# Optimization experiments

Hardware: AMD Instinct MI355X
Metric: run time of the kernel (lower is better)

## Reference

```python
import jax, jax.numpy as jnp
import numpy as np
from jax import lax

B, T = 16384, 1000


def setup_inputs() -> dict:
    key = jax.random.key(0)
    k1, k2, k3, k4 = jax.random.split(key, 4)
    xicovs = jax.random.normal(k1, (B, T, 2, 2), dtype=jnp.float32) * 0.1
    dy = jax.random.normal(k2, (B, T, 2), dtype=jnp.float32) * 0.1
    coeffs_A = jax.random.normal(k3, (2, 2), dtype=jnp.float32) * 0.05
    C = jax.random.normal(k4, (2, 2), dtype=jnp.float32)
    x0 = jnp.zeros((B, 2), dtype=jnp.float32)
    dt = jnp.ones((1,), dtype=jnp.float32) * 0.001
    return {"xicovs": xicovs, "dy": dy, "coeffs_A": coeffs_A, "C": C, "x0": x0, "dt": dt}


def reference(xicovs, dy, coeffs_A, C, x0, dt):
    """Unrolls the GaussianDynamics recurrent cell over T steps with lax.scan.

    Per step (faithful to the original call):
      A_m  = coeffs_A - xicov @ C                     # [B,2,2]
      out  = (C @ x_prev) * dt                        # emitted output
      x    = x_prev + (A_m @ x_prev) * dt + xicov @ dy_t
    Returns (outputs [B,T,2], final_state [B,2]).
    """
    dts = dt[0]

    def step(x, inp):
        xic, dyt = inp  # [B,2,2], [B,2]
        A_m = coeffs_A - jnp.einsum('bij,jk->bik', xic, C)
        out = jnp.einsum('ij,bj->bi', C, x) * dts
        x_new = x + jnp.einsum('bij,bj->bi', A_m, x) * dts + jnp.einsum('bij,bj->bi', xic, dyt)
        return x_new, out

    xs = (jnp.moveaxis(xicovs, 1, 0), jnp.moveaxis(dy, 1, 0))  # time-major
    x_final, outs = lax.scan(step, x0, xs)
    return jnp.moveaxis(outs, 0, 1), x_final
```

## Files before the change

kernel.cpp:

```cpp
#include <hip/hip_runtime.h>


constexpr int BATCH = 16384;
constexpr int TLEN  = 1000;
constexpr int TPB   = 256;
constexpr int SPT   = 4;

typedef float vfloat4 __attribute__((ext_vector_type(4)));
typedef float vfloat2 __attribute__((ext_vector_type(2)));

template <int CTRL, int ROWMASK>
__device__ __forceinline__ float dppf(float oldv, float srcv) {
    return __int_as_float(__builtin_amdgcn_update_dpp(
        __float_as_int(oldv), __float_as_int(srcv), CTRL, ROWMASK, 0xf, false));
}

__global__ __launch_bounds__(TPB, 8) void gd_scan_kernel(
    const float* __restrict__ xicovs,
    const float* __restrict__ dyv,
    const float* __restrict__ cA,
    const float* __restrict__ Cm,
    const float* __restrict__ x0,
    const float* __restrict__ dtp,
    float* __restrict__ out)
{
    __shared__ vfloat4 s_xc[1024];
    __shared__ float wsum[TPB / 64][6];

    const int b    = blockIdx.x;
    const int tid  = threadIdx.x;
    const int lane = tid & 63;
    const int wv   = tid >> 6;

    const int t0  = tid * SPT;
    const int t0m = (t0 <= TLEN - SPT) ? t0 : (TLEN - SPT);

    const float* rowx = xicovs + (size_t)b * TLEN * 4;

#pragma unroll
    for (int k = 0; k < 4; ++k) {
        const int pw = k * 64 + lane;
        const int gw = pw ^ ((pw >> 3) & 7);
        int g = 256 * wv + gw;
        if (g > TLEN - 1) g = TLEN - 1;
        __builtin_amdgcn_global_load_lds(
            (const __attribute__((address_space(1))) void*)(rowx + (size_t)g * 4),
            (__attribute__((address_space(3))) void*)&s_xc[wv * 256 + k * 64],
            16, 0, 0);
    }

    const vfloat4* gd4 = reinterpret_cast<const vfloat4*>(dyv + (size_t)b * TLEN * 2);
    const vfloat4 dA = gd4[(t0m >> 1)];
    const vfloat4 dB = gd4[(t0m >> 1) + 1];

    const float dts = dtp[0];
    const float Cd00 = Cm[0] * dts, Cd01 = Cm[1] * dts, Cd10 = Cm[2] * dts, Cd11 = Cm[3] * dts;
    const float nCd00 = -Cd00, nCd01 = -Cd01, nCd10 = -Cd10, nCd11 = -Cd11;
    const float Ad00 = 1.f + cA[0] * dts, Ad01 = cA[1] * dts;
    const float Ad10 = cA[2] * dts,       Ad11 = 1.f + cA[3] * dts;

    asm volatile("s_waitcnt vmcnt(0)" ::: "memory");

    vfloat4 xc[SPT];
#pragma unroll
    for (int s = 0; s < SPT; ++s) {
        const int gw  = 4 * lane + s;
        const int pos = gw ^ ((gw >> 3) & 7);
        xc[s] = s_xc[wv * 256 + pos];
    }

    const float dy0s[SPT] = {dA.x, dA.z, dB.x, dB.z};
    const float dy1s[SPT] = {dA.y, dA.w, dB.y, dB.w};

    float S00s[SPT], S01s[SPT], S10s[SPT], S11s[SPT], o0s[SPT], o1s[SPT];
    float M00 = 1.f, M01 = 0.f, M10 = 0.f, M11 = 1.f, c0 = 0.f, c1 = 0.f;
#pragma unroll
    for (int s = 0; s < SPT; ++s) {
        const int t = t0 + s;
        const float xi00 = xc[s].x, xi01 = xc[s].y, xi10 = xc[s].z, xi11 = xc[s].w;
        float S00 = Ad00 + xi00 * nCd00 + xi01 * nCd10;
        float S01 = Ad01 + xi00 * nCd01 + xi01 * nCd11;
        float S10 = Ad10 + xi10 * nCd00 + xi11 * nCd10;
        float S11 = Ad11 + xi10 * nCd01 + xi11 * nCd11;
        float o0 = xi00 * dy0s[s] + xi01 * dy1s[s];
        float o1 = xi10 * dy0s[s] + xi11 * dy1s[s];
        if (t >= TLEN) { S00 = 1.f; S01 = 0.f; S10 = 0.f; S11 = 1.f; o0 = 0.f; o1 = 0.f; }
        S00s[s] = S00; S01s[s] = S01; S10s[s] = S10; S11s[s] = S11; o0s[s] = o0; o1s[s] = o1;
        const float n00 = S00 * M00 + S01 * M10;
        const float n01 = S00 * M01 + S01 * M11;
        const float n10 = S10 * M00 + S11 * M10;
        const float n11 = S10 * M01 + S11 * M11;
        const float nc0 = S00 * c0 + S01 * c1 + o0;
        const float nc1 = S10 * c0 + S11 * c1 + o1;
        M00 = n00; M01 = n01; M10 = n10; M11 = n11; c0 = nc0; c1 = nc1;
    }

#define SCAN_STEP(CTRL, RM)                                        \
    do {                                                           \
        const float m00 = dppf<CTRL, RM>(1.f, M00);                \
        const float m01 = dppf<CTRL, RM>(0.f, M01);                \
        const float m10 = dppf<CTRL, RM>(0.f, M10);                \
        const float m11 = dppf<CTRL, RM>(1.f, M11);                \
        const float lc0 = dppf<CTRL, RM>(0.f, c0);                 \
        const float lc1 = dppf<CTRL, RM>(0.f, c1);                 \
        const float n00 = M00 * m00 + M01 * m10;                   \
        const float n01 = M00 * m01 + M01 * m11;                   \
        const float n10 = M10 * m00 + M11 * m10;                   \
        const float n11 = M10 * m01 + M11 * m11;                   \
        const float nc0 = M00 * lc0 + M01 * lc1 + c0;              \
        const float nc1 = M10 * lc0 + M11 * lc1 + c1;              \
        M00 = n00; M01 = n01; M10 = n10; M11 = n11;                \
        c0 = nc0; c1 = nc1;                                        \
    } while (0)

    SCAN_STEP(0x111, 0xf);
    SCAN_STEP(0x112, 0xf);
    SCAN_STEP(0x114, 0xf);
    SCAN_STEP(0x118, 0xf);
    SCAN_STEP(0x142, 0xa);
    SCAN_STEP(0x143, 0xc);
#undef SCAN_STEP

    if (lane == 63) {
        wsum[wv][0] = M00; wsum[wv][1] = M01; wsum[wv][2] = M10; wsum[wv][3] = M11;
        wsum[wv][4] = c0;  wsum[wv][5] = c1;
    }
    __syncthreads();

    float P00 = 1.f, P01 = 0.f, P10 = 0.f, P11 = 1.f, Pc0 = 0.f, Pc1 = 0.f;
    for (int w = 0; w < wv; ++w) {
        const float w00 = wsum[w][0], w01 = wsum[w][1], w10 = wsum[w][2], w11 = wsum[w][3];
        const float wc0 = wsum[w][4], wc1 = wsum[w][5];
        const float n00 = w00 * P00 + w01 * P10;
        const float n01 = w00 * P01 + w01 * P11;
        const float n10 = w10 * P00 + w11 * P10;
        const float n11 = w10 * P01 + w11 * P11;
        const float nc0 = w00 * Pc0 + w01 * Pc1 + wc0;
        const float nc1 = w10 * Pc0 + w11 * Pc1 + wc1;
        P00 = n00; P01 = n01; P10 = n10; P11 = n11; Pc0 = nc0; Pc1 = nc1;
    }

    float e00 = __shfl_up(M00, 1), e01 = __shfl_up(M01, 1);
    float e10 = __shfl_up(M10, 1), e11 = __shfl_up(M11, 1);
    float ec0 = __shfl_up(c0, 1),  ec1 = __shfl_up(c1, 1);
    if (lane == 0) { e00 = 1.f; e01 = 0.f; e10 = 0.f; e11 = 1.f; ec0 = 0.f; ec1 = 0.f; }

    const float E00 = e00 * P00 + e01 * P10;
    const float E01 = e00 * P01 + e01 * P11;
    const float E10 = e10 * P00 + e11 * P10;
    const float E11 = e10 * P01 + e11 * P11;
    const float Ec0 = e00 * Pc0 + e01 * Pc1 + ec0;
    const float Ec1 = e10 * Pc0 + e11 * Pc1 + ec1;

    const float xa = x0[2 * b], xb = x0[2 * b + 1];
    float xq0 = E00 * xa + E01 * xb + Ec0;
    float xq1 = E10 * xa + E11 * xb + Ec1;

    float o0v[SPT], o1v[SPT];
#pragma unroll
    for (int s = 0; s < SPT; ++s) {
        o0v[s] = Cd00 * xq0 + Cd01 * xq1;
        o1v[s] = Cd10 * xq0 + Cd11 * xq1;
        const float nx0 = S00s[s] * xq0 + S01s[s] * xq1 + o0s[s];
        const float nx1 = S10s[s] * xq0 + S11s[s] * xq1 + o1s[s];
        xq0 = nx0; xq1 = nx1;
    }

    float* ob = out + (size_t)b * TLEN * 2 + (size_t)t0 * 2;
    if (t0 + SPT <= TLEN) {
        vfloat4 w0 = {o0v[0], o1v[0], o0v[1], o1v[1]};
        vfloat4 w1 = {o0v[2], o1v[2], o0v[3], o1v[3]};
        __builtin_nontemporal_store(w0, reinterpret_cast<vfloat4*>(ob));
        __builtin_nontemporal_store(w1, reinterpret_cast<vfloat4*>(ob) + 1);
    } else {
        for (int s = 0; s < SPT; ++s)
            if (t0 + s < TLEN) {
                vfloat2 w = {o0v[s], o1v[s]};
                __builtin_nontemporal_store(w, reinterpret_cast<vfloat2*>(ob) + s);
            }
    }

    if (t0 < TLEN && t0 + SPT >= TLEN) {
        float* xf = out + (size_t)BATCH * TLEN * 2 + 2 * b;
        xf[0] = xq0; xf[1] = xq1;
    }
}

extern "C" void kernel_launch(void* const* d_in, const int* in_sizes, int n_in,
                              void* d_out, int out_size, void* d_ws, size_t ws_size,
                              hipStream_t stream) {
    const float* xicovs = (const float*)d_in[0];
    const float* dyv    = (const float*)d_in[1];
    const float* cA     = (const float*)d_in[2];
    const float* Cm     = (const float*)d_in[3];
    const float* x0     = (const float*)d_in[4];
    const float* dtp    = (const float*)d_in[5];
    float* out = (float*)d_out;

    gd_scan_kernel<<<BATCH, TPB, 0, stream>>>(xicovs, dyv, cA, Cm, x0, dtp, out);
}
```

Baseline: 98.81 us.

## Process four rows per block with double-buffered prefetch of next row

Each block now handles four batch rows in sequence, prefetching the next row's xicov tile into a second LDS buffer and its dy values into registers while the current row is scanned. The goal is to hide global load latency and cut per-block launch and setup overhead. Occupancy hint is halved, LDS use doubles, and manual vmcnt waits plus buffer reuse across iterations add risk of races.

```diff
diff --git a/kernel.cpp b/kernel.cpp
--- a/kernel.cpp
+++ b/kernel.cpp
@@ -5,6 +5,8 @@
 constexpr int TLEN  = 1000;
 constexpr int TPB   = 256;
 constexpr int SPT   = 4;
+constexpr int ROWS  = 4;
+constexpr int NBLK  = BATCH / ROWS;
 
 typedef float vfloat4 __attribute__((ext_vector_type(4)));
 typedef float vfloat2 __attribute__((ext_vector_type(2)));
@@ -15,7 +17,7 @@
         __float_as_int(oldv), __float_as_int(srcv), CTRL, ROWMASK, 0xf, false));
 }
 
-__global__ __launch_bounds__(TPB, 8) void gd_scan_kernel(
+__global__ __launch_bounds__(TPB, 4) void gd_scan_kernel(
     const float* __restrict__ xicovs,
     const float* __restrict__ dyv,
     const float* __restrict__ cA,
@@ -24,34 +26,16 @@
     const float* __restrict__ dtp,
     float* __restrict__ out)
 {
-    __shared__ vfloat4 s_xc[1024];
-    __shared__ float wsum[TPB / 64][6];
-
-    const int b    = blockIdx.x;
+    __shared__ vfloat4 s_xc[2][1024];
+    __shared__ float wsum[2][4][6];
+
     const int tid  = threadIdx.x;
     const int lane = tid & 63;
     const int wv   = tid >> 6;
+    const int row0 = blockIdx.x * ROWS;
 
     const int t0  = tid * SPT;
     const int t0m = (t0 <= TLEN - SPT) ? t0 : (TLEN - SPT);
-
-    const float* rowx = xicovs + (size_t)b * TLEN * 4;
-
-#pragma unroll
-    for (int k = 0; k < 4; ++k) {
-        const int pw = k * 64 + lane;
-        const int gw = pw ^ ((pw >> 3) & 7);
-        int g = 256 * wv + gw;
-        if (g > TLEN - 1) g = TLEN - 1;
-        __builtin_amdgcn_global_load_lds(
-            (const __attribute__((address_space(1))) void*)(rowx + (size_t)g * 4),
-            (__attribute__((address_space(3))) void*)&s_xc[wv * 256 + k * 64],
-            16, 0, 0);
-    }
-
-    const vfloat4* gd4 = reinterpret_cast<const vfloat4*>(dyv + (size_t)b * TLEN * 2);
-    const vfloat4 dA = gd4[(t0m >> 1)];
-    const vfloat4 dB = gd4[(t0m >> 1) + 1];
 
     const float dts = dtp[0];
     const float Cd00 = Cm[0] * dts, Cd01 = Cm[1] * dts, Cd10 = Cm[2] * dts, Cd11 = Cm[3] * dts;
@@ -59,131 +43,165 @@
     const float Ad00 = 1.f + cA[0] * dts, Ad01 = cA[1] * dts;
     const float Ad10 = cA[2] * dts,       Ad11 = 1.f + cA[3] * dts;
 
-    asm volatile("s_waitcnt vmcnt(0)" ::: "memory");
-
-    vfloat4 xc[SPT];
-#pragma unroll
-    for (int s = 0; s < SPT; ++s) {
-        const int gw  = 4 * lane + s;
-        const int pos = gw ^ ((gw >> 3) & 7);
-        xc[s] = s_xc[wv * 256 + pos];
+    const vfloat4 x0a = *reinterpret_cast<const vfloat4*>(x0 + (size_t)row0 * 2);
+    const vfloat4 x0b = *reinterpret_cast<const vfloat4*>(x0 + (size_t)row0 * 2 + 4);
+    const float x0s[8] = {x0a.x, x0a.y, x0a.z, x0a.w, x0b.x, x0b.y, x0b.z, x0b.w};
+
+    vfloat4 dyA[2], dyB[2];
+
+#define STAGE(BUF, RR)                                                         \
+    do {                                                                       \
+        const float* rowx_ = xicovs + (size_t)(RR) * (TLEN * 4);               \
+        _Pragma("unroll")                                                      \
+        for (int k = 0; k < 4; ++k) {                                          \
+            const int pw_ = k * 64 + lane;                                     \
+            const int gw_ = pw_ ^ ((pw_ >> 3) & 7);                            \
+            int g_ = 256 * wv + gw_;                                           \
+            if (g_ > TLEN - 1) g_ = TLEN - 1;                                  \
+            __builtin_amdgcn_global_load_lds(                                  \
+                (const __attribute__((address_space(1))) void*)(rowx_ + (size_t)g_ * 4),     \
+                (__attribute__((address_space(3))) void*)&s_xc[BUF][wv * 256 + k * 64],      \
+                16, 0, 0);                                                     \
+        }                                                                      \
+        const vfloat4* gd4_ = reinterpret_cast<const vfloat4*>(dyv + (size_t)(RR) * (TLEN * 2)); \
+        dyA[(RR) & 1] = gd4_[t0m >> 1];                                        \
+        dyB[(RR) & 1] = gd4_[(t0m >> 1) + 1];                                  \
+    } while (0)
+
+    STAGE(0, row0);
+
+#pragma unroll
+    for (int r = 0; r < ROWS; ++r) {
+        const int row = row0 + r;
+        const int buf = r & 1;
+
+        if (r + 1 < ROWS) STAGE((r + 1) & 1, row + 1);
+
+        if (r == 0)            asm volatile("s_waitcnt vmcnt(6)" ::: "memory");
+        else if (r < ROWS - 1) asm volatile("s_waitcnt vmcnt(8)" ::: "memory");
+        else                   asm volatile("s_waitcnt vmcnt(2)" ::: "memory");
+
+        vfloat4 xc[SPT];
+#pragma unroll
+        for (int s = 0; s < SPT; ++s) {
+            const int gw  = 4 * lane + s;
+            const int pos = gw ^ ((gw >> 3) & 7);
+            xc[s] = s_xc[buf][wv * 256 + pos];
+        }
+        const float dy0s[SPT] = {dyA[buf].x, dyA[buf].z, dyB[buf].x, dyB[buf].z};
+        const float dy1s[SPT] = {dyA[buf].y, dyA[buf].w, dyB[buf].y, dyB[buf].w};
+
+        float S00s[SPT], S01s[SPT], S10s[SPT], S11s[SPT], o0s[SPT], o1s[SPT];
+        float M00 = 1.f, M01 = 0.f, M10 = 0.f, M11 = 1.f, c0 = 0.f, c1 = 0.f;
+#pragma unroll
+        for (int s = 0; s < SPT; ++s) {
+            const int t = t0 + s;
+            const float xi00 = xc[s].x, xi01 = xc[s].y, xi10 = xc[s].z, xi11 = xc[s].w;
+            float S00 = Ad00 + xi00 * nCd00 + xi01 * nCd10;
+            float S01 = Ad01 + xi00 * nCd01 + xi01 * nCd11;
+            float S10 = Ad10 + xi10 * nCd00 + xi11 * nCd10;
+            float S11 = Ad11 + xi10 * nCd01 + xi11 * nCd11;
+            float o0 = xi00 * dy0s[s] + xi01 * dy1s[s];
+            float o1 = xi10 * dy0s[s] + xi11 * dy1s[s];
+            if (t >= TLEN) { S00 = 1.f; S01 = 0.f; S10 = 0.f; S11 = 1.f; o0 = 0.f; o1 = 0.f; }
+            S00s[s] = S00; S01s[s] = S01; S10s[s] = S10; S11s[s] = S11; o0s[s] = o0; o1s[s] = o1;
+            const float n00 = S00 * M00 + S01 * M10;
+            const float n01 = S00 * M01 + S01 * M11;
+            const float n10 = S10 * M00 + S11 * M10;
+            const float n11 = S10 * M01 + S11 * M11;
+            const float nc0 = S00 * c0 + S01 * c1 + o0;
+            const float nc1 = S10 * c0 + S11 * c1 + o1;
+            M00 = n00; M01 = n01; M10 = n10; M11 = n11; c0 = nc0; c1 = nc1;
+        }
+
+#define SCAN_STEP(CTRL, RM)                                        \
+        do {                                                       \
+            const float m00 = dppf<CTRL, RM>(1.f, M00);            \
+            const float m01 = dppf<CTRL, RM>(0.f, M01);            \
+            const float m10 = dppf<CTRL, RM>(0.f, M10);            \
+            const float m11 = dppf<CTRL, RM>(1.f, M11);            \
+            const float lc0 = dppf<CTRL, RM>(0.f, c0);             \
+            const float lc1 = dppf<CTRL, RM>(0.f, c1);             \
+            const float n00 = M00 * m00 + M01 * m10;               \
+            const float n01 = M00 * m01 + M01 * m11;               \
+            const float n10 = M10 * m00 + M11 * m10;               \
+            const float n11 = M10 * m01 + M11 * m11;               \
+            const float nc0 = M00 * lc0 + M01 * lc1 + c0;          \
+            const float nc1 = M10 * lc0 + M11 * lc1 + c1;          \
+            M00 = n00; M01 = n01; M10 = n10; M11 = n11;            \
+            c0 = nc0; c1 = nc1;                                    \
+        } while (0)
+
+        SCAN_STEP(0x111, 0xf);
+        SCAN_STEP(0x112, 0xf);
+        SCAN_STEP(0x114, 0xf);
+        SCAN_STEP(0x118, 0xf);
+        SCAN_STEP(0x142, 0xa);
+        SCAN_STEP(0x143, 0xc);
+#undef SCAN_STEP
+
+        if (lane == 63) {
+            wsum[buf][wv][0] = M00; wsum[buf][wv][1] = M01;
+            wsum[buf][wv][2] = M10; wsum[buf][wv][3] = M11;
+            wsum[buf][wv][4] = c0;  wsum[buf][wv][5] = c1;
+        }
+        asm volatile("s_waitcnt lgkmcnt(0)" ::: "memory");
+        __builtin_amdgcn_s_barrier();
+
+        float P00 = 1.f, P01 = 0.f, P10 = 0.f, P11 = 1.f, Pc0 = 0.f, Pc1 = 0.f;
+        for (int w = 0; w < wv; ++w) {
+            const float w00 = wsum[buf][w][0], w01 = wsum[buf][w][1];
+            const float w10 = wsum[buf][w][2], w11 = wsum[buf][w][3];
+            const float wc0 = wsum[buf][w][4], wc1 = wsum[buf][w][5];
+            const float n00 = w00 * P00 + w01 * P10;
+            const float n01 = w00 * P01 + w01 * P11;
+            const float n10 = w10 * P00 + w11 * P10;
+            const float n11 = w10 * P01 + w11 * P11;
+            const float nc0 = w00 * Pc0 + w01 * Pc1 + wc0;
+            const float nc1 = w10 * Pc0 + w11 * Pc1 + wc1;
+            P00 = n00; P01 = n01; P10 = n10; P11 = n11; Pc0 = nc0; Pc1 = nc1;
+        }
+
+        float e00 = __shfl_up(M00, 1), e01 = __shfl_up(M01, 1);
+        float e10 = __shfl_up(M10, 1), e11 = __shfl_up(M11, 1);
+        float ec0 = __shfl_up(c0, 1),  ec1 = __shfl_up(c1, 1);
+        if (lane == 0) { e00 = 1.f; e01 = 0.f; e10 = 0.f; e11 = 1.f; ec0 = 0.f; ec1 = 0.f; }
+
+        const float E00 = e00 * P00 + e01 * P10;
+        const float E01 = e00 * P01 + e01 * P11;
+        const float E10 = e10 * P00 + e11 * P10;
+        const float E11 = e10 * P01 + e11 * P11;
+        const float Ec0 = e00 * Pc0 + e01 * Pc1 + ec0;
+        const float Ec1 = e10 * Pc0 + e11 * Pc1 + ec1;
+
+        const float xa = x0s[2 * r], xb = x0s[2 * r + 1];
+        float xq0 = E00 * xa + E01 * xb + Ec0;
+        float xq1 = E10 * xa + E11 * xb + Ec1;
+
+        float o0v[SPT], o1v[SPT];
+#pragma unroll
+        for (int s = 0; s < SPT; ++s) {
+            o0v[s] = Cd00 * xq0 + Cd01 * xq1;
+            o1v[s] = Cd10 * xq0 + Cd11 * xq1;
+            const float nx0 = S00s[s] * xq0 + S01s[s] * xq1 + o0s[s];
+            const float nx1 = S10s[s] * xq0 + S11s[s] * xq1 + o1s[s];
+            xq0 = nx0; xq1 = nx1;
+        }
+
+        if (t0 < TLEN) {
+            float* ob = out + (size_t)row * TLEN * 2 + (size_t)t0 * 2;
+            vfloat4 w0 = {o0v[0], o1v[0], o0v[1], o1v[1]};
+            vfloat4 w1 = {o0v[2], o1v[2], o0v[3], o1v[3]};
+            __builtin_nontemporal_store(w0, reinterpret_cast<vfloat4*>(ob));
+            __builtin_nontemporal_store(w1, reinterpret_cast<vfloat4*>(ob) + 1);
+        }
+        if (t0 == TLEN - SPT) {
+            vfloat2 xf = {xq0, xq1};
+            __builtin_nontemporal_store(
+                xf, reinterpret_cast<vfloat2*>(out + (size_t)BATCH * TLEN * 2 + 2 * row));
+        }
     }
-
-    const float dy0s[SPT] = {dA.x, dA.z, dB.x, dB.z};
-    const float dy1s[SPT] = {dA.y, dA.w, dB.y, dB.w};
-
-    float S00s[SPT], S01s[SPT], S10s[SPT], S11s[SPT], o0s[SPT], o1s[SPT];
-    float M00 = 1.f, M01 = 0.f, M10 = 0.f, M11 = 1.f, c0 = 0.f, c1 = 0.f;
-#pragma unroll
-    for (int s = 0; s < SPT; ++s) {
-        const int t = t0 + s;
-        const float xi00 = xc[s].x, xi01 = xc[s].y, xi10 = xc[s].z, xi11 = xc[s].w;
-        float S00 = Ad00 + xi00 * nCd00 + xi01 * nCd10;
-        float S01 = Ad01 + xi00 * nCd01 + xi01 * nCd11;
-        float S10 = Ad10 + xi10 * nCd00 + xi11 * nCd10;
-        float S11 = Ad11 + xi10 * nCd01 + xi11 * nCd11;
-        float o0 = xi00 * dy0s[s] + xi01 * dy1s[s];
-        float o1 = xi10 * dy0s[s] + xi11 * dy1s[s];
-        if (t >= TLEN) { S00 = 1.f; S01 = 0.f; S10 = 0.f; S11 = 1.f; o0 = 0.f; o1 = 0.f; }
-        S00s[s] = S00; S01s[s] = S01; S10s[s] = S10; S11s[s] = S11; o0s[s] = o0; o1s[s] = o1;
-        const float n00 = S00 * M00 + S01 * M10;
-        const float n01 = S00 * M01 + S01 * M11;
-        const float n10 = S10 * M00 + S11 * M10;
-        const float n11 = S10 * M01 + S11 * M11;
-        const float nc0 = S00 * c0 + S01 * c1 + o0;
-        const float nc1 = S10 * c0 + S11 * c1 + o1;
-        M00 = n00; M01 = n01; M10 = n10; M11 = n11; c0 = nc0; c1 = nc1;
-    }
-
-#define SCAN_STEP(CTRL, RM)                                        \
-    do {                                                           \
-        const float m00 = dppf<CTRL, RM>(1.f, M00);                \
-        const float m01 = dppf<CTRL, RM>(0.f, M01);                \
-        const float m10 = dppf<CTRL, RM>(0.f, M10);                \
-        const float m11 = dppf<CTRL, RM>(1.f, M11);                \
-        const float lc0 = dppf<CTRL, RM>(0.f, c0);                 \
-        const float lc1 = dppf<CTRL, RM>(0.f, c1);                 \
-        const float n00 = M00 * m00 + M01 * m10;                   \
-        const float n01 = M00 * m01 + M01 * m11;                   \
-        const float n10 = M10 * m00 + M11 * m10;                   \
-        const float n11 = M10 * m01 + M11 * m11;                   \
-        const float nc0 = M00 * lc0 + M01 * lc1 + c0;              \
-        const float nc1 = M10 * lc0 + M11 * lc1 + c1;              \
-        M00 = n00; M01 = n01; M10 = n10; M11 = n11;                \
-        c0 = nc0; c1 = nc1;                                        \
-    } while (0)
-
-    SCAN_STEP(0x111, 0xf);
-    SCAN_STEP(0x112, 0xf);
-    SCAN_STEP(0x114, 0xf);
-    SCAN_STEP(0x118, 0xf);
-    SCAN_STEP(0x142, 0xa);
-    SCAN_STEP(0x143, 0xc);
-#undef SCAN_STEP
-
-    if (lane == 63) {
-        wsum[wv][0] = M00; wsum[wv][1] = M01; wsum[wv][2] = M10; wsum[wv][3] = M11;
-        wsum[wv][4] = c0;  wsum[wv][5] = c1;
-    }
-    __syncthreads();
-
-    float P00 = 1.f, P01 = 0.f, P10 = 0.f, P11 = 1.f, Pc0 = 0.f, Pc1 = 0.f;
-    for (int w = 0; w < wv; ++w) {
-        const float w00 = wsum[w][0], w01 = wsum[w][1], w10 = wsum[w][2], w11 = wsum[w][3];
-        const float wc0 = wsum[w][4], wc1 = wsum[w][5];
-        const float n00 = w00 * P00 + w01 * P10;
-        const float n01 = w00 * P01 + w01 * P11;
-        const float n10 = w10 * P00 + w11 * P10;
-        const float n11 = w10 * P01 + w11 * P11;
-        const float nc0 = w00 * Pc0 + w01 * Pc1 + wc0;
-        const float nc1 = w10 * Pc0 + w11 * Pc1 + wc1;
-        P00 = n00; P01 = n01; P10 = n10; P11 = n11; Pc0 = nc0; Pc1 = nc1;
-    }
-
-    float e00 = __shfl_up(M00, 1), e01 = __shfl_up(M01, 1);
-    float e10 = __shfl_up(M10, 1), e11 = __shfl_up(M11, 1);
-    float ec0 = __shfl_up(c0, 1),  ec1 = __shfl_up(c1, 1);
-    if (lane == 0) { e00 = 1.f; e01 = 0.f; e10 = 0.f; e11 = 1.f; ec0 = 0.f; ec1 = 0.f; }
-
-    const float E00 = e00 * P00 + e01 * P10;
-    const float E01 = e00 * P01 + e01 * P11;
-    const float E10 = e10 * P00 + e11 * P10;
-    const float E11 = e10 * P01 + e11 * P11;
-    const float Ec0 = e00 * Pc0 + e01 * Pc1 + ec0;
-    const float Ec1 = e10 * Pc0 + e11 * Pc1 + ec1;
-
-    const float xa = x0[2 * b], xb = x0[2 * b + 1];
-    float xq0 = E00 * xa + E01 * xb + Ec0;
-    float xq1 = E10 * xa + E11 * xb + Ec1;
-
-    float o0v[SPT], o1v[SPT];
-#pragma unroll
-    for (int s = 0; s < SPT; ++s) {
-        o0v[s] = Cd00 * xq0 + Cd01 * xq1;
-        o1v[s] = Cd10 * xq0 + Cd11 * xq1;
-        const float nx0 = S00s[s] * xq0 + S01s[s] * xq1 + o0s[s];
-        const float nx1 = S10s[s] * xq0 + S11s[s] * xq1 + o1s[s];
-        xq0 = nx0; xq1 = nx1;
-    }
-
-    float* ob = out + (size_t)b * TLEN * 2 + (size_t)t0 * 2;
-    if (t0 + SPT <= TLEN) {
-        vfloat4 w0 = {o0v[0], o1v[0], o0v[1], o1v[1]};
-        vfloat4 w1 = {o0v[2], o1v[2], o0v[3], o1v[3]};
-        __builtin_nontemporal_store(w0, reinterpret_cast<vfloat4*>(ob));
-        __builtin_nontemporal_store(w1, reinterpret_cast<vfloat4*>(ob) + 1);
-    } else {
-        for (int s = 0; s < SPT; ++s)
-            if (t0 + s < TLEN) {
-                vfloat2 w = {o0v[s], o1v[s]};
-                __builtin_nontemporal_store(w, reinterpret_cast<vfloat2*>(ob) + s);
-            }
-    }
-
-    if (t0 < TLEN && t0 + SPT >= TLEN) {
-        float* xf = out + (size_t)BATCH * TLEN * 2 + 2 * b;
-        xf[0] = xq0; xf[1] = xq1;
-    }
+#undef STAGE
 }
 
 extern "C" void kernel_launch(void* const* d_in, const int* in_sizes, int n_in,
@@ -197,5 +215,5 @@
     const float* dtp    = (const float*)d_in[5];
     float* out = (float*)d_out;
 
-    gd_scan_kernel<<<BATCH, TPB, 0, stream>>>(xicovs, dyv, cA, Cm, x0, dtp, out);
+    gd_scan_kernel<<<NBLK, TPB, 0, stream>>>(xicovs, dyv, cA, Cm, x0, dtp, out);
 }
```

Result: slower. 112.8 us (+14.1%).

## Process two batch rows per block with eight timesteps per thread

Applied to the files above, without the earlier changes.

Each 256-thread block now handles two batch rows, so each row gets 128 threads, and each thread covers eight timesteps instead of four. The cross-wave combine shrinks to a single carry from wave 0 to wave 1 per row, and the block count is halved. The LDS swizzle is reworked for the new layout, and only 125 of every 128 threads do real work. The intent is to cut the serial cross-wave prefix and per-block overhead. In exchange, per-thread register use rises and launch bounds drop to 4 blocks per CU.

```diff
diff --git a/kernel.cpp b/kernel.cpp
--- a/kernel.cpp
+++ b/kernel.cpp
@@ -4,7 +4,9 @@
 constexpr int BATCH = 16384;
 constexpr int TLEN  = 1000;
 constexpr int TPB   = 256;
-constexpr int SPT   = 4;
+constexpr int SPT   = 8;
+constexpr int RPB   = 2;
+constexpr int NBLK  = BATCH / RPB;
 
 typedef float vfloat4 __attribute__((ext_vector_type(4)));
 typedef float vfloat2 __attribute__((ext_vector_type(2)));
@@ -15,7 +17,7 @@
         __float_as_int(oldv), __float_as_int(srcv), CTRL, ROWMASK, 0xf, false));
 }
 
-__global__ __launch_bounds__(TPB, 8) void gd_scan_kernel(
+__global__ __launch_bounds__(TPB, 4) void gd_scan_kernel(
     const float* __restrict__ xicovs,
     const float* __restrict__ dyv,
     const float* __restrict__ cA,
@@ -24,67 +26,65 @@
     const float* __restrict__ dtp,
     float* __restrict__ out)
 {
-    __shared__ vfloat4 s_xc[1024];
-    __shared__ float wsum[TPB / 64][6];
+    __shared__ vfloat4 s_xc[RPB][1024];
+    __shared__ float wsum[RPB][6];
 
-    const int b    = blockIdx.x;
     const int tid  = threadIdx.x;
     const int lane = tid & 63;
-    const int wv   = tid >> 6;
+    const int rb   = tid >> 7;
+    const int w01  = (tid >> 6) & 1;
+    const int r    = tid & 127;
+    const int row  = blockIdx.x * RPB + rb;
+    const bool valid = (r < 125);
 
-    const int t0  = tid * SPT;
-    const int t0m = (t0 <= TLEN - SPT) ? t0 : (TLEN - SPT);
-
-    const float* rowx = xicovs + (size_t)b * TLEN * 4;
-
+    {
+        const float* rowx = xicovs + (size_t)row * (TLEN * 4);
 #pragma unroll
-    for (int k = 0; k < 4; ++k) {
-        const int pw = k * 64 + lane;
-        const int gw = pw ^ ((pw >> 3) & 7);
-        int g = 256 * wv + gw;
-        if (g > TLEN - 1) g = TLEN - 1;
-        __builtin_amdgcn_global_load_lds(
-            (const __attribute__((address_space(1))) void*)(rowx + (size_t)g * 4),
-            (__attribute__((address_space(3))) void*)&s_xc[wv * 256 + k * 64],
-            16, 0, 0);
+        for (int k = 0; k < 8; ++k) {
+            const int p  = k * 64 + lane;
+            int g = 512 * w01 + (p ^ ((p >> 3) & 7));
+            if (g > TLEN - 1) g = TLEN - 1;
+            __builtin_amdgcn_global_load_lds(
+                (const __attribute__((address_space(1))) void*)(rowx + (size_t)g * 4),
+                (__attribute__((address_space(3))) void*)&s_xc[rb][512 * w01 + k * 64],
+                16, 0, 0);
+        }
     }
 
-    const vfloat4* gd4 = reinterpret_cast<const vfloat4*>(dyv + (size_t)b * TLEN * 2);
-    const vfloat4 dA = gd4[(t0m >> 1)];
-    const vfloat4 dB = gd4[(t0m >> 1) + 1];
+    const int rbase = valid ? r : 124;
+    const vfloat4* gd4 = reinterpret_cast<const vfloat4*>(
+        dyv + (size_t)row * (TLEN * 2) + (size_t)rbase * 16);
+    const vfloat4 d0 = gd4[0], d1 = gd4[1], d2 = gd4[2], d3 = gd4[3];
 
     const float dts = dtp[0];
     const float Cd00 = Cm[0] * dts, Cd01 = Cm[1] * dts, Cd10 = Cm[2] * dts, Cd11 = Cm[3] * dts;
     const float nCd00 = -Cd00, nCd01 = -Cd01, nCd10 = -Cd10, nCd11 = -Cd11;
     const float Ad00 = 1.f + cA[0] * dts, Ad01 = cA[1] * dts;
     const float Ad10 = cA[2] * dts,       Ad11 = 1.f + cA[3] * dts;
+    const float xa = x0[2 * row], xb = x0[2 * row + 1];
 
     asm volatile("s_waitcnt vmcnt(0)" ::: "memory");
 
     vfloat4 xc[SPT];
 #pragma unroll
     for (int s = 0; s < SPT; ++s) {
-        const int gw  = 4 * lane + s;
-        const int pos = gw ^ ((gw >> 3) & 7);
-        xc[s] = s_xc[wv * 256 + pos];
+        const int pos = 8 * r + (s ^ (r & 7));
+        xc[s] = s_xc[rb][pos];
     }
-
-    const float dy0s[SPT] = {dA.x, dA.z, dB.x, dB.z};
-    const float dy1s[SPT] = {dA.y, dA.w, dB.y, dB.w};
+    const float dy0s[SPT] = {d0.x, d0.z, d1.x, d1.z, d2.x, d2.z, d3.x, d3.z};
+    const float dy1s[SPT] = {d0.y, d0.w, d1.y, d1.w, d2.y, d2.w, d3.y, d3.w};
 
     float S00s[SPT], S01s[SPT], S10s[SPT], S11s[SPT], o0s[SPT], o1s[SPT];
     float M00 = 1.f, M01 = 0.f, M10 = 0.f, M11 = 1.f, c0 = 0.f, c1 = 0.f;
 #pragma unroll
     for (int s = 0; s < SPT; ++s) {
-        const int t = t0 + s;
         const float xi00 = xc[s].x, xi01 = xc[s].y, xi10 = xc[s].z, xi11 = xc[s].w;
-        float S00 = Ad00 + xi00 * nCd00 + xi01 * nCd10;
-        float S01 = Ad01 + xi00 * nCd01 + xi01 * nCd11;
-        float S10 = Ad10 + xi10 * nCd00 + xi11 * nCd10;
-        float S11 = Ad11 + xi10 * nCd01 + xi11 * nCd11;
-        float o0 = xi00 * dy0s[s] + xi01 * dy1s[s];
-        float o1 = xi10 * dy0s[s] + xi11 * dy1s[s];
-        if (t >= TLEN) { S00 = 1.f; S01 = 0.f; S10 = 0.f; S11 = 1.f; o0 = 0.f; o1 = 0.f; }
+        const float S00 = Ad00 + xi00 * nCd00 + xi01 * nCd10;
+        const float S01 = Ad01 + xi00 * nCd01 + xi01 * nCd11;
+        const float S10 = Ad10 + xi10 * nCd00 + xi11 * nCd10;
+        const float S11 = Ad11 + xi10 * nCd01 + xi11 * nCd11;
+        const float o0 = xi00 * dy0s[s] + xi01 * dy1s[s];
+        const float o1 = xi10 * dy0s[s] + xi11 * dy1s[s];
         S00s[s] = S00; S01s[s] = S01; S10s[s] = S10; S11s[s] = S11; o0s[s] = o0; o1s[s] = o1;
         const float n00 = S00 * M00 + S01 * M10;
         const float n01 = S00 * M01 + S01 * M11;
@@ -94,6 +94,7 @@
         const float nc1 = S10 * c0 + S11 * c1 + o1;
         M00 = n00; M01 = n01; M10 = n10; M11 = n11; c0 = nc0; c1 = nc1;
     }
+    if (!valid) { M00 = 1.f; M01 = 0.f; M10 = 0.f; M11 = 1.f; c0 = 0.f; c1 = 0.f; }
 
 #define SCAN_STEP(CTRL, RM)                                        \
     do {                                                           \
@@ -121,23 +122,16 @@
     SCAN_STEP(0x143, 0xc);
 #undef SCAN_STEP
 
-    if (lane == 63) {
-        wsum[wv][0] = M00; wsum[wv][1] = M01; wsum[wv][2] = M10; wsum[wv][3] = M11;
-        wsum[wv][4] = c0;  wsum[wv][5] = c1;
+    if (w01 == 0 && lane == 63) {
+        wsum[rb][0] = M00; wsum[rb][1] = M01; wsum[rb][2] = M10; wsum[rb][3] = M11;
+        wsum[rb][4] = c0;  wsum[rb][5] = c1;
     }
     __syncthreads();
 
     float P00 = 1.f, P01 = 0.f, P10 = 0.f, P11 = 1.f, Pc0 = 0.f, Pc1 = 0.f;
-    for (int w = 0; w < wv; ++w) {
-        const float w00 = wsum[w][0], w01 = wsum[w][1], w10 = wsum[w][2], w11 = wsum[w][3];
-        const float wc0 = wsum[w][4], wc1 = wsum[w][5];
-        const float n00 = w00 * P00 + w01 * P10;
-        const float n01 = w00 * P01 + w01 * P11;
-        const float n10 = w10 * P00 + w11 * P10;
-        const float n11 = w10 * P01 + w11 * P11;
-        const float nc0 = w00 * Pc0 + w01 * Pc1 + wc0;
-        const float nc1 = w10 * Pc0 + w11 * Pc1 + wc1;
-        P00 = n00; P01 = n01; P10 = n10; P11 = n11; Pc0 = nc0; Pc1 = nc1;
+    if (w01) {
+        P00 = wsum[rb][0]; P01 = wsum[rb][1]; P10 = wsum[rb][2]; P11 = wsum[rb][3];
+        Pc0 = wsum[rb][4]; Pc1 = wsum[rb][5];
     }
 
     float e00 = __shfl_up(M00, 1), e01 = __shfl_up(M01, 1);
@@ -152,7 +146,6 @@
     const float Ec0 = e00 * Pc0 + e01 * Pc1 + ec0;
     const float Ec1 = e10 * Pc0 + e11 * Pc1 + ec1;
 
-    const float xa = x0[2 * b], xb = x0[2 * b + 1];
     float xq0 = E00 * xa + E01 * xb + Ec0;
     float xq1 = E10 * xa + E11 * xb + Ec1;
 
@@ -166,23 +159,21 @@
         xq0 = nx0; xq1 = nx1;
     }
 
-    float* ob = out + (size_t)b * TLEN * 2 + (size_t)t0 * 2;
-    if (t0 + SPT <= TLEN) {
+    if (valid) {
+        float* ob = out + (size_t)row * (TLEN * 2) + (size_t)r * 16;
         vfloat4 w0 = {o0v[0], o1v[0], o0v[1], o1v[1]};
         vfloat4 w1 = {o0v[2], o1v[2], o0v[3], o1v[3]};
+        vfloat4 w2 = {o0v[4], o1v[4], o0v[5], o1v[5]};
+        vfloat4 w3 = {o0v[6], o1v[6], o0v[7], o1v[7]};
         __builtin_nontemporal_store(w0, reinterpret_cast<vfloat4*>(ob));
         __builtin_nontemporal_store(w1, reinterpret_cast<vfloat4*>(ob) + 1);
-    } else {
-        for (int s = 0; s < SPT; ++s)
-            if (t0 + s < TLEN) {
-                vfloat2 w = {o0v[s], o1v[s]};
-                __builtin_nontemporal_store(w, reinterpret_cast<vfloat2*>(ob) + s);
-            }
+        __builtin_nontemporal_store(w2, reinterpret_cast<vfloat4*>(ob) + 2);
+        __builtin_nontemporal_store(w3, reinterpret_cast<vfloat4*>(ob) + 3);
     }
-
-    if (t0 < TLEN && t0 + SPT >= TLEN) {
-        float* xf = out + (size_t)BATCH * TLEN * 2 + 2 * b;
-        xf[0] = xq0; xf[1] = xq1;
+    if (r == 124) {
+        vfloat2 xf = {xq0, xq1};
+        __builtin_nontemporal_store(
+            xf, reinterpret_cast<vfloat2*>(out + (size_t)BATCH * (TLEN * 2) + 2 * row));
     }
 }
 
@@ -197,5 +188,5 @@
     const float* dtp    = (const float*)d_in[5];
     float* out = (float*)d_out;
 
-    gd_scan_kernel<<<BATCH, TPB, 0, stream>>>(xicovs, dyv, cA, Cm, x0, dtp, out);
+    gd_scan_kernel<<<NBLK, TPB, 0, stream>>>(xicovs, dyv, cA, Cm, x0, dtp, out);
 }
```

Measured after the change: 173.9 us. 1.76x slower.
